# Kernel tuning notes

Hardware: AMD Instinct MI355X
Metric: run time of the kernel (lower is better)

Reference implementation:

```python
import jax, jax.numpy as jnp
import numpy as np

WEIGHT = 1.0


def _smooth_l1(pred, target):
    # F.smooth_l1_loss default: beta=1.0, reduction='mean'
    d = jnp.abs(pred - target)
    loss = jnp.where(d < 1.0, 0.5 * d * d, d - 0.5)
    return jnp.mean(loss)


def setup_inputs() -> dict:
    key = jax.random.key(0)
    k0, k1, k2 = jax.random.split(key, 3)
    B, L = 4096, 128
    return {
        "outputs0": jax.random.normal(k0, (B, B), dtype=jnp.float32),
        "outputs1": jax.random.normal(k1, (B, B), dtype=jnp.float32),
        "labels": jax.random.normal(k2, (B, L), dtype=jnp.float32),
    }


def reference(outputs0, outputs1, labels):
    # vector = [labels | ones]  -> [B, 2L]
    ones = jnp.ones_like(labels)
    vector = jnp.concatenate([labels, ones], axis=1)
    cos1 = vector @ vector.T                                   # [B, B]
    mod = jnp.sqrt(jnp.sum(vector * vector, axis=1, keepdims=True))  # [B, 1]
    cos2 = mod @ mod.T                                         # [B, B]
    multi_labels = jnp.floor(cos1 / cos2)                      # on-device floor (replaces cpu/numpy roundtrip)
    total_loss = (_smooth_l1(outputs0, multi_labels) + _smooth_l1(outputs1, multi_labels)) / 2.0
    return WEIGHT * total_loss
```

## Files before the change

### kernel.cpp

```cpp
#include <hip/hip_runtime.h>
#include <hip/hip_bf16.h>

#define B_N 4096
#define L_K 128
#define NBLK ((B_N / 64) * (B_N / 64))

typedef __bf16 bf16x8 __attribute__((ext_vector_type(8)));
typedef float  f32x4  __attribute__((ext_vector_type(4)));

__global__ __launch_bounds__(256) void prep_kernel(const float* __restrict__ labels,
                                                   unsigned short* __restrict__ lb,
                                                   float* __restrict__ inv) {
    const int wave = blockIdx.x * 4 + (threadIdx.x >> 6);
    const int lane = threadIdx.x & 63;
    const int row  = wave;

    const float x0 = labels[row * L_K + lane];
    const float x1 = labels[row * L_K + 64 + lane];

    __hip_bfloat16 h0 = __float2bfloat16(x0);
    __hip_bfloat16 h1 = __float2bfloat16(x1);
    lb[row * L_K + lane]      = *reinterpret_cast<unsigned short*>(&h0);
    lb[row * L_K + 64 + lane] = *reinterpret_cast<unsigned short*>(&h1);

    float s = x0 * x0 + x1 * x1;
    #pragma unroll
    for (int m = 32; m >= 1; m >>= 1) s += __shfl_xor(s, m);
    if (lane == 0) inv[row] = 1.0f / sqrtf(s + 128.0f);
}

__global__ __launch_bounds__(256) void main_kernel(const float* __restrict__ o0,
                                                   const float* __restrict__ o1,
                                                   const unsigned short* __restrict__ lb,
                                                   const float* __restrict__ inv,
                                                   float* __restrict__ partials) {
    __shared__ __align__(16) float m_lds[64][64];
    __shared__ float wsum[4];

    const int ti = blockIdx.x >> 6;
    const int tj = blockIdx.x & 63;
    const int w  = threadIdx.x >> 6;
    const int l  = threadIdx.x & 63;
    const int fr = l & 15;
    const int fk = (l >> 4) * 8;

    const int r0 = ti * 64 + w * 16;
    const int c0 = tj * 64;

    f32x4 acc[4] = {};

    #pragma unroll
    for (int kk = 0; kk < 4; ++kk) {
        const bf16x8 a = *reinterpret_cast<const bf16x8*>(
            lb + (size_t)(r0 + fr) * L_K + kk * 32 + fk);
        #pragma unroll
        for (int ct = 0; ct < 4; ++ct) {
            const bf16x8 b = *reinterpret_cast<const bf16x8*>(
                lb + (size_t)(c0 + ct * 16 + fr) * L_K + kk * 32 + fk);
            acc[ct] = __builtin_amdgcn_mfma_f32_16x16x32_bf16(a, b, acc[ct], 0, 0, 0);
        }
    }

    float invi[4];
    #pragma unroll
    for (int r = 0; r < 4; ++r) invi[r] = inv[r0 + (l >> 4) * 4 + r];
    float invj[4];
    #pragma unroll
    for (int ct = 0; ct < 4; ++ct) invj[ct] = inv[c0 + ct * 16 + (l & 15)];

    #pragma unroll
    for (int ct = 0; ct < 4; ++ct) {
        #pragma unroll
        for (int r = 0; r < 4; ++r) {
            const int li = w * 16 + (l >> 4) * 4 + r;
            const int lj = ct * 16 + (l & 15);
            const float ratio = (acc[ct][r] + 128.0f) * invi[r] * invj[ct];
            m_lds[li][lj] = floorf(ratio);
        }
    }
    __syncthreads();

    float lsum = 0.0f;
    #pragma unroll
    for (int v = 0; v < 4; ++v) {
        const int idx = v * 256 + threadIdx.x;
        const int row = idx >> 4;
        const int c4  = (idx & 15) * 4;
        const size_t goff = (size_t)(ti * 64 + row) * B_N + (size_t)(tj * 64 + c4);
        const float4 a0 = *reinterpret_cast<const float4*>(o0 + goff);
        const float4 a1 = *reinterpret_cast<const float4*>(o1 + goff);
        const float4 mm = *reinterpret_cast<const float4*>(&m_lds[row][c4]);

        const float mv[4] = {mm.x, mm.y, mm.z, mm.w};
        const float p0[4] = {a0.x, a0.y, a0.z, a0.w};
        const float p1[4] = {a1.x, a1.y, a1.z, a1.w};
        #pragma unroll
        for (int q = 0; q < 4; ++q) {
            float d0 = fabsf(p0[q] - mv[q]);
            float d1 = fabsf(p1[q] - mv[q]);
            lsum += (d0 < 1.0f) ? 0.5f * d0 * d0 : d0 - 0.5f;
            lsum += (d1 < 1.0f) ? 0.5f * d1 * d1 : d1 - 0.5f;
        }
    }

    #pragma unroll
    for (int m = 32; m >= 1; m >>= 1) lsum += __shfl_xor(lsum, m);
    if (l == 0) wsum[w] = lsum;
    __syncthreads();
    if (threadIdx.x == 0)
        partials[blockIdx.x] = wsum[0] + wsum[1] + wsum[2] + wsum[3];
}

__global__ __launch_bounds__(1024) void fin_kernel(const float* __restrict__ partials,
                                                   float* __restrict__ out) {
    __shared__ double wred[16];
    double s = 0.0;
    for (int i = threadIdx.x; i < NBLK; i += 1024) s += (double)partials[i];
    #pragma unroll
    for (int m = 32; m >= 1; m >>= 1) s += __shfl_xor(s, m);
    const int l = threadIdx.x & 63, w = threadIdx.x >> 6;
    if (l == 0) wred[w] = s;
    __syncthreads();
    if (threadIdx.x == 0) {
        double t = 0.0;
        #pragma unroll
        for (int i = 0; i < 16; ++i) t += wred[i];
        out[0] = (float)(t / (2.0 * (double)B_N * (double)B_N));
    }
}

extern "C" void kernel_launch(void* const* d_in, const int* in_sizes, int n_in,
                              void* d_out, int out_size, void* d_ws, size_t ws_size,
                              hipStream_t stream) {
    const float* o0     = (const float*)d_in[0];
    const float* o1     = (const float*)d_in[1];
    const float* labels = (const float*)d_in[2];
    float* out = (float*)d_out;

    char* ws = (char*)d_ws;
    unsigned short* lb = (unsigned short*)ws;
    float* inv      = (float*)(ws + (size_t)B_N * L_K * 2);
    float* partials = (float*)(ws + (size_t)B_N * L_K * 2 + B_N * 4);

    prep_kernel<<<B_N / 4, 256, 0, stream>>>(labels, lb, inv);
    main_kernel<<<NBLK, 256, 0, stream>>>(o0, o1, lb, inv, partials);
    fin_kernel<<<1, 1024, 0, stream>>>(partials, out);
}
```

Baseline: 184.3 us.

## Prefetch output tiles into LDS via async global_load_lds before MFMA

At kernel start, each block issues direct global-to-LDS loads for its 64x64 tiles of outputs0 and outputs1. The MFMA Gram computation and floor step then run while those loads are in flight, and the smooth-L1 pass reads both tiles from LDS. The loads of the inverse norms are also moved ahead of the MFMA loop. This is meant to hide the DRAM latency of the dominant streaming reads behind compute. In exchange, LDS use per block triples, which may reduce how many blocks fit on each CU, and correctness depends on the LDS DMA completing before the barrier.

```diff
diff --git a/kernel.cpp b/kernel.cpp
--- a/kernel.cpp
+++ b/kernel.cpp
@@ -7,6 +7,9 @@
 
 typedef __bf16 bf16x8 __attribute__((ext_vector_type(8)));
 typedef float  f32x4  __attribute__((ext_vector_type(4)));
+
+#define GPTR(p) (const __attribute__((address_space(1))) void*)(p)
+#define LPTR(p) (__attribute__((address_space(3))) void*)(p)
 
 __global__ __launch_bounds__(256) void prep_kernel(const float* __restrict__ labels,
                                                    unsigned short* __restrict__ lb,
@@ -34,6 +37,8 @@
                                                    const unsigned short* __restrict__ lb,
                                                    const float* __restrict__ inv,
                                                    float* __restrict__ partials) {
+    __shared__ __align__(16) float o0t[64 * 64];
+    __shared__ __align__(16) float o1t[64 * 64];
     __shared__ __align__(16) float m_lds[64][64];
     __shared__ float wsum[4];
 
@@ -41,14 +46,33 @@
     const int tj = blockIdx.x & 63;
     const int w  = threadIdx.x >> 6;
     const int l  = threadIdx.x & 63;
+
+    {
+        const int sr = l >> 4;
+        const int sc = (l & 15) * 4;
+        #pragma unroll
+        for (int q2 = 0; q2 < 4; ++q2) {
+            const int q   = w * 4 + q2;
+            const int row = q * 4 + sr;
+            const size_t goff = (size_t)(ti * 64 + row) * B_N + (size_t)(tj * 64 + sc);
+            __builtin_amdgcn_global_load_lds(GPTR(o0 + goff), LPTR(&o0t[q * 256]), 16, 0, 0);
+            __builtin_amdgcn_global_load_lds(GPTR(o1 + goff), LPTR(&o1t[q * 256]), 16, 0, 0);
+        }
+    }
+
     const int fr = l & 15;
     const int fk = (l >> 4) * 8;
-
     const int r0 = ti * 64 + w * 16;
     const int c0 = tj * 64;
 
+    float invi[4];
+    #pragma unroll
+    for (int r = 0; r < 4; ++r) invi[r] = inv[r0 + (l >> 4) * 4 + r];
+    float invj[4];
+    #pragma unroll
+    for (int ct = 0; ct < 4; ++ct) invj[ct] = inv[c0 + ct * 16 + (l & 15)];
+
     f32x4 acc[4] = {};
-
     #pragma unroll
     for (int kk = 0; kk < 4; ++kk) {
         const bf16x8 a = *reinterpret_cast<const bf16x8*>(
@@ -61,13 +85,6 @@
         }
     }
 
-    float invi[4];
-    #pragma unroll
-    for (int r = 0; r < 4; ++r) invi[r] = inv[r0 + (l >> 4) * 4 + r];
-    float invj[4];
-    #pragma unroll
-    for (int ct = 0; ct < 4; ++ct) invj[ct] = inv[c0 + ct * 16 + (l & 15)];
-
     #pragma unroll
     for (int ct = 0; ct < 4; ++ct) {
         #pragma unroll
@@ -78,6 +95,7 @@
             m_lds[li][lj] = floorf(ratio);
         }
     }
+
     __syncthreads();
 
     float lsum = 0.0f;
@@ -86,18 +104,13 @@
         const int idx = v * 256 + threadIdx.x;
         const int row = idx >> 4;
         const int c4  = (idx & 15) * 4;
-        const size_t goff = (size_t)(ti * 64 + row) * B_N + (size_t)(tj * 64 + c4);
-        const float4 a0 = *reinterpret_cast<const float4*>(o0 + goff);
-        const float4 a1 = *reinterpret_cast<const float4*>(o1 + goff);
-        const float4 mm = *reinterpret_cast<const float4*>(&m_lds[row][c4]);
-
-        const float mv[4] = {mm.x, mm.y, mm.z, mm.w};
-        const float p0[4] = {a0.x, a0.y, a0.z, a0.w};
-        const float p1[4] = {a1.x, a1.y, a1.z, a1.w};
+        const f32x4 a0 = *reinterpret_cast<const f32x4*>(&o0t[row * 64 + c4]);
+        const f32x4 a1 = *reinterpret_cast<const f32x4*>(&o1t[row * 64 + c4]);
+        const f32x4 mm = *reinterpret_cast<const f32x4*>(&m_lds[row][c4]);
         #pragma unroll
         for (int q = 0; q < 4; ++q) {
-            float d0 = fabsf(p0[q] - mv[q]);
-            float d1 = fabsf(p1[q] - mv[q]);
+            float d0 = fabsf(a0[q] - mm[q]);
+            float d1 = fabsf(a1[q] - mm[q]);
             lsum += (d0 < 1.0f) ? 0.5f * d0 * d0 : d0 - 0.5f;
             lsum += (d1 < 1.0f) ? 0.5f * d1 * d1 : d1 - 0.5f;
         }
```

After: 165.8 us. -10.0%, faster.

## Give each wave a 16x256 strip, drop LDS staging, use branchless smooth-L1

Applied to the files above, without the earlier changes.

Each wave now owns an independent 16-row by 256-column strip. It keeps its A fragments in registers across four 64-column sub-tiles and reads the outputs straight from global memory in MFMA accumulator layout, so there is no LDS round trip and no block barriers. The smooth-L1 branch becomes a min/max form, with 0.5*min^2 + max - 1 and the constant subtracted per wave. The grid shrinks to 1024 blocks. The cost is uncoalesced scalar global loads, 16 consecutive floats per row segment instead of float4, in a kernel that is bandwidth-bound.

```diff
diff --git a/kernel.cpp b/kernel.cpp
--- a/kernel.cpp
+++ b/kernel.cpp
@@ -3,7 +3,7 @@
 
 #define B_N 4096
 #define L_K 128
-#define NBLK ((B_N / 64) * (B_N / 64))
+#define NPART 4096
 
 typedef __bf16 bf16x8 __attribute__((ext_vector_type(8)));
 typedef float  f32x4  __attribute__((ext_vector_type(4)));
@@ -34,88 +34,86 @@
                                                    const unsigned short* __restrict__ lb,
                                                    const float* __restrict__ inv,
                                                    float* __restrict__ partials) {
-    __shared__ __align__(16) float m_lds[64][64];
-    __shared__ float wsum[4];
+    const int w = threadIdx.x >> 6;
+    const int l = threadIdx.x & 63;
+    const int task = blockIdx.x * 4 + w;
+    const int s = task >> 4;
+    const int q = task & 15;
 
-    const int ti = blockIdx.x >> 6;
-    const int tj = blockIdx.x & 63;
-    const int w  = threadIdx.x >> 6;
-    const int l  = threadIdx.x & 63;
     const int fr = l & 15;
     const int fk = (l >> 4) * 8;
+    const int r0 = s * 16;
+    const int rr = (l >> 4) * 4;
 
-    const int r0 = ti * 64 + w * 16;
-    const int c0 = tj * 64;
+    bf16x8 a[4];
+    #pragma unroll
+    for (int kk = 0; kk < 4; ++kk)
+        a[kk] = *reinterpret_cast<const bf16x8*>(
+            lb + (size_t)(r0 + fr) * L_K + kk * 32 + fk);
 
-    f32x4 acc[4] = {};
+    float invi[4];
+    #pragma unroll
+    for (int r = 0; r < 4; ++r) invi[r] = inv[r0 + rr + r];
+
+    float sumA = 0.0f, sumB = 0.0f;
 
     #pragma unroll
-    for (int kk = 0; kk < 4; ++kk) {
-        const bf16x8 a = *reinterpret_cast<const bf16x8*>(
-            lb + (size_t)(r0 + fr) * L_K + kk * 32 + fk);
+    for (int t = 0; t < 4; ++t) {
+        const int c0 = q * 256 + t * 64;
+
+        f32x4 acc[4] = {};
+        #pragma unroll
+        for (int kk = 0; kk < 4; ++kk) {
+            #pragma unroll
+            for (int ct = 0; ct < 4; ++ct) {
+                const bf16x8 b = *reinterpret_cast<const bf16x8*>(
+                    lb + (size_t)(c0 + ct * 16 + fr) * L_K + kk * 32 + fk);
+                acc[ct] = __builtin_amdgcn_mfma_f32_16x16x32_bf16(a[kk], b, acc[ct], 0, 0, 0);
+            }
+        }
+
+        float p0v[16], p1v[16];
+        #pragma unroll
+        for (int r = 0; r < 4; ++r) {
+            const size_t rowoff = (size_t)(r0 + rr + r) * B_N + (size_t)(c0 + fr);
+            #pragma unroll
+            for (int ct = 0; ct < 4; ++ct) {
+                p0v[r * 4 + ct] = o0[rowoff + ct * 16];
+                p1v[r * 4 + ct] = o1[rowoff + ct * 16];
+            }
+        }
+
+        float invj[4];
+        #pragma unroll
+        for (int ct = 0; ct < 4; ++ct) invj[ct] = inv[c0 + ct * 16 + fr];
+
         #pragma unroll
         for (int ct = 0; ct < 4; ++ct) {
-            const bf16x8 b = *reinterpret_cast<const bf16x8*>(
-                lb + (size_t)(c0 + ct * 16 + fr) * L_K + kk * 32 + fk);
-            acc[ct] = __builtin_amdgcn_mfma_f32_16x16x32_bf16(a, b, acc[ct], 0, 0, 0);
+            #pragma unroll
+            for (int r = 0; r < 4; ++r) {
+                const float m  = floorf((acc[ct][r] + 128.0f) * invi[r] * invj[ct]);
+                const float d0 = fabsf(p0v[r * 4 + ct] - m);
+                const float d1 = fabsf(p1v[r * 4 + ct] - m);
+                const float u0 = fminf(d0, 1.0f), v0 = fmaxf(d0, 1.0f);
+                const float u1 = fminf(d1, 1.0f), v1 = fmaxf(d1, 1.0f);
+                sumA = fmaf(u0, u0, sumA);
+                sumA = fmaf(u1, u1, sumA);
+                sumB += v0 + v1;
+            }
         }
     }
 
-    float invi[4];
-    #pragma unroll
-    for (int r = 0; r < 4; ++r) invi[r] = inv[r0 + (l >> 4) * 4 + r];
-    float invj[4];
-    #pragma unroll
-    for (int ct = 0; ct < 4; ++ct) invj[ct] = inv[c0 + ct * 16 + (l & 15)];
-
-    #pragma unroll
-    for (int ct = 0; ct < 4; ++ct) {
-        #pragma unroll
-        for (int r = 0; r < 4; ++r) {
-            const int li = w * 16 + (l >> 4) * 4 + r;
-            const int lj = ct * 16 + (l & 15);
-            const float ratio = (acc[ct][r] + 128.0f) * invi[r] * invj[ct];
-            m_lds[li][lj] = floorf(ratio);
-        }
-    }
-    __syncthreads();
-
-    float lsum = 0.0f;
-    #pragma unroll
-    for (int v = 0; v < 4; ++v) {
-        const int idx = v * 256 + threadIdx.x;
-        const int row = idx >> 4;
-        const int c4  = (idx & 15) * 4;
-        const size_t goff = (size_t)(ti * 64 + row) * B_N + (size_t)(tj * 64 + c4);
-        const float4 a0 = *reinterpret_cast<const float4*>(o0 + goff);
-        const float4 a1 = *reinterpret_cast<const float4*>(o1 + goff);
-        const float4 mm = *reinterpret_cast<const float4*>(&m_lds[row][c4]);
-
-        const float mv[4] = {mm.x, mm.y, mm.z, mm.w};
-        const float p0[4] = {a0.x, a0.y, a0.z, a0.w};
-        const float p1[4] = {a1.x, a1.y, a1.z, a1.w};
-        #pragma unroll
-        for (int q = 0; q < 4; ++q) {
-            float d0 = fabsf(p0[q] - mv[q]);
-            float d1 = fabsf(p1[q] - mv[q]);
-            lsum += (d0 < 1.0f) ? 0.5f * d0 * d0 : d0 - 0.5f;
-            lsum += (d1 < 1.0f) ? 0.5f * d1 * d1 : d1 - 0.5f;
-        }
-    }
-
+    float lsum = 0.5f * sumA + sumB;
     #pragma unroll
     for (int m = 32; m >= 1; m >>= 1) lsum += __shfl_xor(lsum, m);
-    if (l == 0) wsum[w] = lsum;
-    __syncthreads();
-    if (threadIdx.x == 0)
-        partials[blockIdx.x] = wsum[0] + wsum[1] + wsum[2] + wsum[3];
+    if (l == 0) partials[task] = lsum - 8192.0f;
 }
 
 __global__ __launch_bounds__(1024) void fin_kernel(const float* __restrict__ partials,
                                                    float* __restrict__ out) {
     __shared__ double wred[16];
     double s = 0.0;
-    for (int i = threadIdx.x; i < NBLK; i += 1024) s += (double)partials[i];
+    for (int i = threadIdx.x; i < NPART; i += 1024) s += (double)partials[i];
     #pragma unroll
     for (int m = 32; m >= 1; m >>= 1) s += __shfl_xor(s, m);
     const int l = threadIdx.x & 63, w = threadIdx.x >> 6;
@@ -143,6 +141,6 @@
     float* partials = (float*)(ws + (size_t)B_N * L_K * 2 + B_N * 4);
 
     prep_kernel<<<B_N / 4, 256, 0, stream>>>(labels, lb, inv);
-    main_kernel<<<NBLK, 256, 0, stream>>>(o0, o1, lb, inv, partials);
+    main_kernel<<<NPART / 4, 256, 0, stream>>>(o0, o1, lb, inv, partials);
     fin_kernel<<<1, 1024, 0, stream>>>(partials, out);
 }
```

New measurement: 177.1 us. 1.04x faster.
